# Kernel optimization log

Measured on AMD Instinct MI355X. Metric: run time of the kernel, lower is better.

Reference implementation:

```python
import jax, jax.numpy as jnp
import numpy as np

H, D, DS, CZ, S, B = 16, 24, 384, 128, 512, 1
EPS = 1e-5


def setup_inputs() -> dict:
    key = jax.random.key(0)
    ks = jax.random.split(key, 12)
    sc = lambda fan: 1.0 / np.sqrt(fan)
    inp = {
        's': jax.random.normal(ks[0], (B, S, DS), jnp.float32),
        'z': jax.random.normal(ks[1], (B, S, S, CZ), jnp.float32),
        'seq_mask': jnp.zeros((B, 1, 1, S), jnp.float32),
        'q_w': jax.random.normal(ks[2], (H * D, DS), jnp.float32) * sc(DS),
        'q_b': jax.random.normal(ks[3], (H * D,), jnp.float32) * 0.02,
        'k_w': jax.random.normal(ks[4], (H * D, DS), jnp.float32) * sc(DS),
        'v_w': jax.random.normal(ks[5], (H * D, DS), jnp.float32) * sc(DS),
        'g_w': jax.random.normal(ks[6], (H * D, DS), jnp.float32) * sc(DS),
        'o_w': jax.random.normal(ks[7], (DS, H * D), jnp.float32) * sc(H * D),
        'z_ln_w': jnp.ones((CZ,), jnp.float32),
        'z_ln_b': jnp.zeros((CZ,), jnp.float32),
        'z_w': jax.random.normal(ks[8], (H, CZ), jnp.float32) * sc(CZ),
    }
    return inp


def _layer_norm(x, w, b):
    mu = jnp.mean(x, axis=-1, keepdims=True)
    var = jnp.mean(jnp.square(x - mu), axis=-1, keepdims=True)
    return (x - mu) * jax.lax.rsqrt(var + EPS) * w + b


def reference(s, z, seq_mask, q_w, q_b, k_w, v_w, g_w, o_w, z_ln_w, z_ln_b, z_w):
    b, n, _ = s.shape
    # fused QKV projection (q has bias, k/v do not)
    q = (s @ q_w.T + q_b).reshape(b, n, H, D).transpose(0, 2, 1, 3)  # [B,H,S,D]
    k = (s @ k_w.T).reshape(b, n, H, D).transpose(0, 2, 1, 3)
    v = (s @ v_w.T).reshape(b, n, H, D).transpose(0, 2, 1, 3)
    # pair bias: layernorm(z) -> linear to H -> permute to [B,H,S,S]
    bias = _layer_norm(z, z_ln_w, z_ln_b) @ z_w.T          # [B,S,S,H]
    bias = bias.transpose(0, 3, 1, 2)                      # [B,H,S,S]
    bias = bias + seq_mask
    scores = jnp.einsum('bhqd,bhkd->bhqk', q, k) * (D ** -0.5) + bias
    attn = jax.nn.softmax(scores, axis=-1)
    o = jnp.einsum('bhqk,bhkd->bhqd', attn, v)             # [B,H,S,D]
    o = o.transpose(0, 2, 1, 3).reshape(b, n, H * D)
    g = jax.nn.sigmoid(s @ g_w.T)                          # gating
    return (o * g) @ o_w.T                                 # [B,S,DS]
```

## Files before the change

kernel.cpp:

```cpp
#include <hip/hip_runtime.h>

#define H 16
#define D 24
#define DS 384
#define CZ 128
#define S 512
#define EPSV 1e-5f

__global__ __launch_bounds__(256) void proj_kernel(
    const float* __restrict__ s, const float* __restrict__ q_w, const float* __restrict__ q_b,
    const float* __restrict__ k_w, const float* __restrict__ v_w, const float* __restrict__ g_w,
    float* __restrict__ Q, float* __restrict__ K, float* __restrict__ V, float* __restrict__ G)
{
    const int b = blockIdx.x;
    const int mat = b / 48;
    const int t = b % 48;
    const int by = t / 6, bx = t % 6;
    const float* w = (mat == 0) ? q_w : (mat == 1) ? k_w : (mat == 2) ? v_w : g_w;

    __shared__ float As[32][68];
    __shared__ float Ws[32][68];

    const int tid = threadIdx.x;
    const int tx = tid & 15, ty = tid >> 4;
    const int r8 = tid >> 3;
    const int c4 = tid & 7;

    float acc[4][4] = {};
    for (int kc = 0; kc < DS; kc += 32) {
        __syncthreads();
#pragma unroll
        for (int pass = 0; pass < 2; ++pass) {
            int r = r8 + pass * 32;
            float4 sv = *(const float4*)(s + (by * 64 + r) * DS + kc + c4 * 4);
            float4 wv = *(const float4*)(w + (bx * 64 + r) * DS + kc + c4 * 4);
            As[c4 * 4 + 0][r] = sv.x; As[c4 * 4 + 1][r] = sv.y;
            As[c4 * 4 + 2][r] = sv.z; As[c4 * 4 + 3][r] = sv.w;
            Ws[c4 * 4 + 0][r] = wv.x; Ws[c4 * 4 + 1][r] = wv.y;
            Ws[c4 * 4 + 2][r] = wv.z; Ws[c4 * 4 + 3][r] = wv.w;
        }
        __syncthreads();
#pragma unroll
        for (int k = 0; k < 32; ++k) {
            float4 a4 = *(const float4*)&As[k][ty * 4];
            float4 b4 = *(const float4*)&Ws[k][tx * 4];
            acc[0][0] += a4.x * b4.x; acc[0][1] += a4.x * b4.y; acc[0][2] += a4.x * b4.z; acc[0][3] += a4.x * b4.w;
            acc[1][0] += a4.y * b4.x; acc[1][1] += a4.y * b4.y; acc[1][2] += a4.y * b4.z; acc[1][3] += a4.y * b4.w;
            acc[2][0] += a4.z * b4.x; acc[2][1] += a4.z * b4.y; acc[2][2] += a4.z * b4.z; acc[2][3] += a4.z * b4.w;
            acc[3][0] += a4.w * b4.x; acc[3][1] += a4.w * b4.y; acc[3][2] += a4.w * b4.z; acc[3][3] += a4.w * b4.w;
        }
    }

    const int r0 = by * 64 + ty * 4;
    const int c0 = bx * 64 + tx * 4;
    float* dst = (mat == 0) ? Q : (mat == 1) ? K : (mat == 2) ? V : G;
#pragma unroll
    for (int ii = 0; ii < 4; ++ii) {
        float4 v;
        v.x = acc[ii][0]; v.y = acc[ii][1]; v.z = acc[ii][2]; v.w = acc[ii][3];
        if (mat == 0) {
            v.x += q_b[c0 + 0]; v.y += q_b[c0 + 1]; v.z += q_b[c0 + 2]; v.w += q_b[c0 + 3];
        } else if (mat == 3) {
            v.x = 1.f / (1.f + __expf(-v.x)); v.y = 1.f / (1.f + __expf(-v.y));
            v.z = 1.f / (1.f + __expf(-v.z)); v.w = 1.f / (1.f + __expf(-v.w));
        }
        *(float4*)(dst + (r0 + ii) * DS + c0) = v;
    }
}

__global__ __launch_bounds__(256) void score_kernel(
    const float* __restrict__ z, const float* __restrict__ seq_mask,
    const float* __restrict__ z_ln_w, const float* __restrict__ z_ln_b,
    const float* __restrict__ z_w,
    const float* __restrict__ Q, const float* __restrict__ K,
    float* __restrict__ scores)
{
    const int b = blockIdx.x;
    const int q = b >> 3;
    const int j0 = (b & 7) * 64;
    const int tid = threadIdx.x;
    const int w = tid >> 6;
    const int lane = tid & 63;

    __shared__ float a_s[H][CZ + 4];
    __shared__ float AhBh[2][H];
    __shared__ float qrow[DS];
    __shared__ float stats[4][2][68];
    __shared__ float opart[4][H][68];
    __shared__ float buf[H][68];

    {
        const int h = tid >> 4;
        const int c8 = (tid & 15) * 8;
        float A = 0.f, Bv = 0.f;
#pragma unroll
        for (int p = 0; p < 2; ++p) {
            float4 wz = *(const float4*)(z_w + h * CZ + c8 + p * 4);
            float4 lw = *(const float4*)(z_ln_w + c8 + p * 4);
            float4 lb = *(const float4*)(z_ln_b + c8 + p * 4);
            float4 a;
            a.x = lw.x * wz.x; a.y = lw.y * wz.y; a.z = lw.z * wz.z; a.w = lw.w * wz.w;
            *(float4*)&a_s[h][c8 + p * 4] = a;
            A += a.x + a.y + a.z + a.w;
            Bv += lb.x * wz.x + lb.y * wz.y + lb.z * wz.z + lb.w * wz.w;
        }
#pragma unroll
        for (int m = 1; m < 16; m <<= 1) {
            A += __shfl_xor(A, m);
            Bv += __shfl_xor(Bv, m);
        }
        if ((tid & 15) == 0) { AhBh[0][h] = A; AhBh[1][h] = Bv; }
    }
    for (int i = tid; i < DS; i += 256) qrow[i] = Q[q * DS + i];
    __syncthreads();

    {
        const int c0 = w * 32;
        const float* zr = z + ((long)q * S + j0 + lane) * CZ + c0;
        float4 zf[8];
#pragma unroll
        for (int t = 0; t < 8; ++t) zf[t] = *(const float4*)(zr + t * 4);

        float s1 = 0.f, s2 = 0.f;
#pragma unroll
        for (int t = 0; t < 8; ++t) {
            s1 += zf[t].x + zf[t].y + zf[t].z + zf[t].w;
            s2 += zf[t].x * zf[t].x + zf[t].y * zf[t].y + zf[t].z * zf[t].z + zf[t].w * zf[t].w;
        }
        stats[w][0][lane] = s1;
        stats[w][1][lane] = s2;

#pragma unroll
        for (int h = 0; h < H; ++h) {
            float acc = 0.f;
#pragma unroll
            for (int t = 0; t < 8; ++t) {
                float4 a4 = *(const float4*)&a_s[h][c0 + t * 4];
                acc += zf[t].x * a4.x + zf[t].y * a4.y + zf[t].z * a4.z + zf[t].w * a4.w;
            }
            opart[w][h][lane] = acc;
        }
    }
    __syncthreads();

    {
        const int r = tid >> 2;
        const int hq = tid & 3;
        float s1 = stats[0][0][r] + stats[1][0][r] + stats[2][0][r] + stats[3][0][r];
        float s2 = stats[0][1][r] + stats[1][1][r] + stats[2][1][r] + stats[3][1][r];
        const float mu = s1 * (1.f / 128.f);
        const float rs = rsqrtf(s2 * (1.f / 128.f) - mu * mu + EPSV);
        const float mk = seq_mask[j0 + r];
        const float scale = 0.2041241452319315f;
        const float* krow = K + (long)(j0 + r) * DS;

#pragma unroll
        for (int i = 0; i < 4; ++i) {
            const int h = hq * 4 + i;
            float dza = opart[0][h][r] + opart[1][h][r] + opart[2][h][r] + opart[3][h][r];
            const float4* k4 = (const float4*)(krow + h * D);
            const float4* q4 = (const float4*)(qrow + h * D);
            float qk = 0.f;
#pragma unroll
            for (int t = 0; t < 6; ++t) {
                float4 kv = k4[t];
                float4 qv = q4[t];
                qk += kv.x * qv.x + kv.y * qv.y + kv.z * qv.z + kv.w * qv.w;
            }
            const float bias = rs * dza - mu * rs * AhBh[0][h] + AhBh[1][h];
            buf[h][r] = qk * scale + bias + mk;
        }
    }
    __syncthreads();

    {
        const int h = tid >> 4, j4 = tid & 15;
        float4 v = *(const float4*)&buf[h][j4 * 4];
        *(float4*)(scores + ((q << 4) + h) * S + j0 + j4 * 4) = v;
    }
}

__global__ __launch_bounds__(256) void spv_kernel(
    const float* __restrict__ scores, const float* __restrict__ V,
    const float* __restrict__ G, float* __restrict__ og)
{
    const int q = blockIdx.x;
    const int tid = threadIdx.x;
    const int wv = tid >> 6;
    const int lane = tid & 63;

    __shared__ float sc[H][S + 4];
    __shared__ float opart[4][DS];
    __shared__ float inv_l[H];

    for (int i = tid; i < H * (S / 4); i += 256) {
        int row = i >> 7, f4 = i & 127;
        float4 v = ((const float4*)(scores + ((q << 4) + row) * S))[f4];
        *(float4*)&sc[row][f4 * 4] = v;
    }
    __syncthreads();

#pragma unroll
    for (int i = 0; i < 4; ++i) {
        int h = wv * 4 + i;
        float m = -1e30f;
        for (int j = lane; j < S; j += 64) m = fmaxf(m, sc[h][j]);
#pragma unroll
        for (int mk = 1; mk < 64; mk <<= 1) m = fmaxf(m, __shfl_xor(m, mk));
        float sum = 0.f;
        for (int j = lane; j < S; j += 64) {
            float p = __expf(sc[h][j] - m);
            sc[h][j] = p;
            sum += p;
        }
#pragma unroll
        for (int mk = 1; mk < 64; mk <<= 1) sum += __shfl_xor(sum, mk);
        if (lane == 0) inv_l[h] = 1.f / sum;
    }
    __syncthreads();

    {
        const int jb = wv * 128;
        const int c0 = lane * 4;
        const int h0 = c0 / 24;
        const int c1 = 256 + lane * 4;
        const int h1 = c1 / 24;
        float4 a0 = {0.f, 0.f, 0.f, 0.f};
        float4 a1 = {0.f, 0.f, 0.f, 0.f};
#pragma unroll 4
        for (int jj = 0; jj < 128; ++jj) {
            const int j = jb + jj;
            const float4* vr = (const float4*)(V + (long)j * DS);
            const float p0 = sc[h0][j];
            float4 v0 = vr[lane];
            a0.x += p0 * v0.x; a0.y += p0 * v0.y; a0.z += p0 * v0.z; a0.w += p0 * v0.w;
            if (lane < 32) {
                const float p1 = sc[h1][j];
                float4 v1 = vr[64 + lane];
                a1.x += p1 * v1.x; a1.y += p1 * v1.y; a1.z += p1 * v1.z; a1.w += p1 * v1.w;
            }
        }
        *(float4*)&opart[wv][c0] = a0;
        if (lane < 32) *(float4*)&opart[wv][c1] = a1;
    }
    __syncthreads();
    for (int i = tid; i < DS; i += 256) {
        float o = opart[0][i] + opart[1][i] + opart[2][i] + opart[3][i];
        int h = i / 24;
        og[q * DS + i] = o * inv_l[h] * G[q * DS + i];
    }
}

__global__ __launch_bounds__(256) void out_kernel(
    const float* __restrict__ og, const float* __restrict__ o_w, float* __restrict__ out)
{
    const int b = blockIdx.x;
    const int by = b / 6, bx = b % 6;

    __shared__ float As[32][68];
    __shared__ float Ws[32][68];

    const int tid = threadIdx.x;
    const int tx = tid & 15, ty = tid >> 4;
    const int r8 = tid >> 3;
    const int c4 = tid & 7;

    float acc[4][4] = {};
    for (int kc = 0; kc < DS; kc += 32) {
        __syncthreads();
#pragma unroll
        for (int pass = 0; pass < 2; ++pass) {
            int r = r8 + pass * 32;
            float4 sv = *(const float4*)(og + (by * 64 + r) * DS + kc + c4 * 4);
            float4 wvv = *(const float4*)(o_w + (bx * 64 + r) * DS + kc + c4 * 4);
            As[c4 * 4 + 0][r] = sv.x; As[c4 * 4 + 1][r] = sv.y;
            As[c4 * 4 + 2][r] = sv.z; As[c4 * 4 + 3][r] = sv.w;
            Ws[c4 * 4 + 0][r] = wvv.x; Ws[c4 * 4 + 1][r] = wvv.y;
            Ws[c4 * 4 + 2][r] = wvv.z; Ws[c4 * 4 + 3][r] = wvv.w;
        }
        __syncthreads();
#pragma unroll
        for (int k = 0; k < 32; ++k) {
            float4 a4 = *(const float4*)&As[k][ty * 4];
            float4 b4 = *(const float4*)&Ws[k][tx * 4];
            acc[0][0] += a4.x * b4.x; acc[0][1] += a4.x * b4.y; acc[0][2] += a4.x * b4.z; acc[0][3] += a4.x * b4.w;
            acc[1][0] += a4.y * b4.x; acc[1][1] += a4.y * b4.y; acc[1][2] += a4.y * b4.z; acc[1][3] += a4.y * b4.w;
            acc[2][0] += a4.z * b4.x; acc[2][1] += a4.z * b4.y; acc[2][2] += a4.z * b4.z; acc[2][3] += a4.z * b4.w;
            acc[3][0] += a4.w * b4.x; acc[3][1] += a4.w * b4.y; acc[3][2] += a4.w * b4.z; acc[3][3] += a4.w * b4.w;
        }
    }

    const int r0 = by * 64 + ty * 4;
    const int c0 = bx * 64 + tx * 4;
#pragma unroll
    for (int ii = 0; ii < 4; ++ii) {
        float4 v;
        v.x = acc[ii][0]; v.y = acc[ii][1]; v.z = acc[ii][2]; v.w = acc[ii][3];
        *(float4*)(out + (r0 + ii) * DS + c0) = v;
    }
}

extern "C" void kernel_launch(void* const* d_in, const int* in_sizes, int n_in,
                              void* d_out, int out_size, void* d_ws, size_t ws_size,
                              hipStream_t stream)
{
    const float* s      = (const float*)d_in[0];
    const float* z      = (const float*)d_in[1];
    const float* mask   = (const float*)d_in[2];
    const float* q_w    = (const float*)d_in[3];
    const float* q_b    = (const float*)d_in[4];
    const float* k_w    = (const float*)d_in[5];
    const float* v_w    = (const float*)d_in[6];
    const float* g_w    = (const float*)d_in[7];
    const float* o_w    = (const float*)d_in[8];
    const float* z_ln_w = (const float*)d_in[9];
    const float* z_ln_b = (const float*)d_in[10];
    const float* z_w    = (const float*)d_in[11];

    float* Q  = (float*)d_ws;
    float* K  = Q + S * DS;
    float* V  = K + S * DS;
    float* G  = V + S * DS;
    float* og = G + S * DS;
    float* scores = og + S * DS;

    hipLaunchKernelGGL(proj_kernel, dim3(192), dim3(256), 0, stream,
                       s, q_w, q_b, k_w, v_w, g_w, Q, K, V, G);
    hipLaunchKernelGGL(score_kernel, dim3(4096), dim3(256), 0, stream,
                       z, mask, z_ln_w, z_ln_b, z_w, Q, K, scores);
    hipLaunchKernelGGL(spv_kernel, dim3(S), dim3(256), 0, stream,
                       scores, V, G, og);
    hipLaunchKernelGGL(out_kernel, dim3(48), dim3(256), 0, stream,
                       og, o_w, (float*)d_out);
}
```

Measured before the change: 338.2 us.

## Restructure score kernel to stage z tiles in shared memory with register-blocked heads

The score kernel now handles 128 key rows per block instead of 64, halving the grid. Each block streams z through shared memory in 32-channel chunks. Each thread computes 4 heads for 2 rows, keeping the LN-folded weights in registers and accumulating layernorm statistics and the bias projection directly, so the cross-wave partial-sum reductions through shared memory go away. Q is read straight from global memory rather than staged. The kernel now needs more synchronisation per chunk and more registers, and the halved grid lowers parallelism.

```diff
diff --git a/kernel.cpp b/kernel.cpp
--- a/kernel.cpp
+++ b/kernel.cpp
@@ -76,18 +76,15 @@
     float* __restrict__ scores)
 {
     const int b = blockIdx.x;
-    const int q = b >> 3;
-    const int j0 = (b & 7) * 64;
+    const int q = b >> 2;
+    const int j0 = (b & 3) * 128;
     const int tid = threadIdx.x;
-    const int w = tid >> 6;
-    const int lane = tid & 63;
+    const int r = tid >> 2;
+    const int hq = tid & 3;
 
     __shared__ float a_s[H][CZ + 4];
     __shared__ float AhBh[2][H];
-    __shared__ float qrow[DS];
-    __shared__ float stats[4][2][68];
-    __shared__ float opart[4][H][68];
-    __shared__ float buf[H][68];
+    __shared__ float zs[128 * 36];
 
     {
         const int h = tid >> 4;
@@ -111,71 +108,105 @@
         }
         if ((tid & 15) == 0) { AhBh[0][h] = A; AhBh[1][h] = Bv; }
     }
-    for (int i = tid; i < DS; i += 256) qrow[i] = Q[q * DS + i];
-    __syncthreads();
-
-    {
-        const int c0 = w * 32;
-        const float* zr = z + ((long)q * S + j0 + lane) * CZ + c0;
-        float4 zf[8];
-#pragma unroll
-        for (int t = 0; t < 8; ++t) zf[t] = *(const float4*)(zr + t * 4);
-
-        float s1 = 0.f, s2 = 0.f;
-#pragma unroll
-        for (int t = 0; t < 8; ++t) {
-            s1 += zf[t].x + zf[t].y + zf[t].z + zf[t].w;
-            s2 += zf[t].x * zf[t].x + zf[t].y * zf[t].y + zf[t].z * zf[t].z + zf[t].w * zf[t].w;
-        }
-        stats[w][0][lane] = s1;
-        stats[w][1][lane] = s2;
-
-#pragma unroll
-        for (int h = 0; h < H; ++h) {
-            float acc = 0.f;
-#pragma unroll
-            for (int t = 0; t < 8; ++t) {
-                float4 a4 = *(const float4*)&a_s[h][c0 + t * 4];
-                acc += zf[t].x * a4.x + zf[t].y * a4.y + zf[t].z * a4.z + zf[t].w * a4.w;
+    __syncthreads();
+
+    float accz[2][4] = {};
+    float s1[2] = {0.f, 0.f}, s2[2] = {0.f, 0.f};
+    const float* zq = z + ((long)q * S + j0) * CZ;
+
+    for (int cc = 0; cc < 4; ++cc) {
+        const int c0 = cc * 32;
+#pragma unroll
+        for (int it = 0; it < 4; ++it) {
+            const int idx = it * 256 + tid;
+            const int row = idx >> 3, c8 = idx & 7;
+            float4 v = *(const float4*)(zq + (long)row * CZ + c0 + c8 * 4);
+            *(float4*)&zs[row * 36 + c8 * 4] = v;
+        }
+        __syncthreads();
+
+#pragma unroll
+        for (int sub = 0; sub < 2; ++sub) {
+            const int cb = sub * 16;
+            float4 areg[4][4];
+#pragma unroll
+            for (int i = 0; i < 4; ++i)
+#pragma unroll
+                for (int t = 0; t < 4; ++t)
+                    areg[i][t] = *(const float4*)&a_s[hq * 4 + i][c0 + cb + t * 4];
+
+#pragma unroll
+            for (int tl = 0; tl < 2; ++tl) {
+                const int row = tl * 64 + r;
+                float4 zf[4];
+#pragma unroll
+                for (int t = 0; t < 4; ++t)
+                    zf[t] = *(const float4*)&zs[row * 36 + cb + t * 4];
+#pragma unroll
+                for (int t = 0; t < 4; ++t) {
+                    s1[tl] += zf[t].x + zf[t].y + zf[t].z + zf[t].w;
+                    s2[tl] += zf[t].x * zf[t].x + zf[t].y * zf[t].y
+                            + zf[t].z * zf[t].z + zf[t].w * zf[t].w;
+                }
+#pragma unroll
+                for (int i = 0; i < 4; ++i) {
+                    accz[tl][i] += zf[0].x * areg[i][0].x + zf[0].y * areg[i][0].y
+                                 + zf[0].z * areg[i][0].z + zf[0].w * areg[i][0].w
+                                 + zf[1].x * areg[i][1].x + zf[1].y * areg[i][1].y
+                                 + zf[1].z * areg[i][1].z + zf[1].w * areg[i][1].w
+                                 + zf[2].x * areg[i][2].x + zf[2].y * areg[i][2].y
+                                 + zf[2].z * areg[i][2].z + zf[2].w * areg[i][2].w
+                                 + zf[3].x * areg[i][3].x + zf[3].y * areg[i][3].y
+                                 + zf[3].z * areg[i][3].z + zf[3].w * areg[i][3].w;
+                }
             }
-            opart[w][h][lane] = acc;
-        }
-    }
-    __syncthreads();
-
-    {
-        const int r = tid >> 2;
-        const int hq = tid & 3;
-        float s1 = stats[0][0][r] + stats[1][0][r] + stats[2][0][r] + stats[3][0][r];
-        float s2 = stats[0][1][r] + stats[1][1][r] + stats[2][1][r] + stats[3][1][r];
-        const float mu = s1 * (1.f / 128.f);
-        const float rs = rsqrtf(s2 * (1.f / 128.f) - mu * mu + EPSV);
-        const float mk = seq_mask[j0 + r];
-        const float scale = 0.2041241452319315f;
-        const float* krow = K + (long)(j0 + r) * DS;
-
+        }
+        __syncthreads();
+    }
+
+    float qk[2][4];
+#pragma unroll
+    for (int i = 0; i < 4; ++i) {
+        const int h = hq * 4 + i;
+        float4 qreg[6];
+#pragma unroll
+        for (int t = 0; t < 6; ++t)
+            qreg[t] = *(const float4*)(Q + q * DS + h * D + t * 4);
+#pragma unroll
+        for (int tl = 0; tl < 2; ++tl) {
+            const float4* kp = (const float4*)(K + (long)(j0 + tl * 64 + r) * DS + h * D);
+            float a = 0.f;
+#pragma unroll
+            for (int t = 0; t < 6; ++t) {
+                float4 kv = kp[t];
+                a += kv.x * qreg[t].x + kv.y * qreg[t].y + kv.z * qreg[t].z + kv.w * qreg[t].w;
+            }
+            qk[tl][i] = a;
+        }
+    }
+
+    float* buf = zs;
+    const float scale = 0.2041241452319315f;
+#pragma unroll
+    for (int tl = 0; tl < 2; ++tl) {
+        const int row = tl * 64 + r;
+        const float mu = s1[tl] * (1.f / 128.f);
+        const float rs = rsqrtf(s2[tl] * (1.f / 128.f) - mu * mu + EPSV);
+        const float mk = seq_mask[j0 + row];
 #pragma unroll
         for (int i = 0; i < 4; ++i) {
             const int h = hq * 4 + i;
-            float dza = opart[0][h][r] + opart[1][h][r] + opart[2][h][r] + opart[3][h][r];
-            const float4* k4 = (const float4*)(krow + h * D);
-            const float4* q4 = (const float4*)(qrow + h * D);
-            float qk = 0.f;
-#pragma unroll
-            for (int t = 0; t < 6; ++t) {
-                float4 kv = k4[t];
-                float4 qv = q4[t];
-                qk += kv.x * qv.x + kv.y * qv.y + kv.z * qv.z + kv.w * qv.w;
-            }
-            const float bias = rs * dza - mu * rs * AhBh[0][h] + AhBh[1][h];
-            buf[h][r] = qk * scale + bias + mk;
-        }
-    }
-    __syncthreads();
-
-    {
-        const int h = tid >> 4, j4 = tid & 15;
-        float4 v = *(const float4*)&buf[h][j4 * 4];
+            const float bias = rs * accz[tl][i] - mu * rs * AhBh[0][h] + AhBh[1][h];
+            buf[h * 132 + row] = qk[tl][i] * scale + bias + mk;
+        }
+    }
+    __syncthreads();
+
+#pragma unroll
+    for (int it = 0; it < 2; ++it) {
+        const int idx = it * 256 + tid;
+        const int h = idx >> 5, j4 = idx & 31;
+        float4 v = *(const float4*)&buf[h * 132 + j4 * 4];
         *(float4*)(scores + ((q << 4) + h) * S + j0 + j4 * 4) = v;
     }
 }
@@ -326,7 +357,7 @@
 
     hipLaunchKernelGGL(proj_kernel, dim3(192), dim3(256), 0, stream,
                        s, q_w, q_b, k_w, v_w, g_w, Q, K, V, G);
-    hipLaunchKernelGGL(score_kernel, dim3(4096), dim3(256), 0, stream,
+    hipLaunchKernelGGL(score_kernel, dim3(2048), dim3(256), 0, stream,
                        z, mask, z_ln_w, z_ln_b, z_w, Q, K, scores);
     hipLaunchKernelGGL(spv_kernel, dim3(S), dim3(256), 0, stream,
                        scores, V, G, og);
```

Result: slower. 383.8 us (+13.5%).

## Reduce pair-bias partial sums with wave shuffles instead of shared memory

Applied to the files above, without the earlier changes.

Reassigns work in the score kernel so the four lanes covering one z row sit together in a wave, each handling 32 channels. The layernorm statistics and per-head dot products are combined with xor shuffles, which removes the stats and opart shared arrays and one block barrier. Q is read straight from global memory instead of being staged in shared memory. The cost is 16 extra registers per thread for the per-head partials and a less coalesced z load pattern, since each lane now reads a 128-byte chunk from a different row.

```diff
diff --git a/kernel.cpp b/kernel.cpp
--- a/kernel.cpp
+++ b/kernel.cpp
@@ -81,12 +81,12 @@
     const int tid = threadIdx.x;
     const int w = tid >> 6;
     const int lane = tid & 63;
-
-    __shared__ float a_s[H][CZ + 4];
+    const int r = lane >> 2;
+    const int c = lane & 3;
+    const int row = w * 16 + r;
+
+    __shared__ float a_s[H][4][36];
     __shared__ float AhBh[2][H];
-    __shared__ float qrow[DS];
-    __shared__ float stats[4][2][68];
-    __shared__ float opart[4][H][68];
     __shared__ float buf[H][68];
 
     {
@@ -95,12 +95,13 @@
         float A = 0.f, Bv = 0.f;
 #pragma unroll
         for (int p = 0; p < 2; ++p) {
-            float4 wz = *(const float4*)(z_w + h * CZ + c8 + p * 4);
-            float4 lw = *(const float4*)(z_ln_w + c8 + p * 4);
-            float4 lb = *(const float4*)(z_ln_b + c8 + p * 4);
+            const int ch = c8 + p * 4;
+            float4 wz = *(const float4*)(z_w + h * CZ + ch);
+            float4 lw = *(const float4*)(z_ln_w + ch);
+            float4 lb = *(const float4*)(z_ln_b + ch);
             float4 a;
             a.x = lw.x * wz.x; a.y = lw.y * wz.y; a.z = lw.z * wz.z; a.w = lw.w * wz.w;
-            *(float4*)&a_s[h][c8 + p * 4] = a;
+            *(float4*)&a_s[h][ch >> 5][ch & 31] = a;
             A += a.x + a.y + a.z + a.w;
             Bv += lb.x * wz.x + lb.y * wz.y + lb.z * wz.z + lb.w * wz.w;
         }
@@ -111,65 +112,59 @@
         }
         if ((tid & 15) == 0) { AhBh[0][h] = A; AhBh[1][h] = Bv; }
     }
-    for (int i = tid; i < DS; i += 256) qrow[i] = Q[q * DS + i];
-    __syncthreads();
-
-    {
-        const int c0 = w * 32;
-        const float* zr = z + ((long)q * S + j0 + lane) * CZ + c0;
-        float4 zf[8];
-#pragma unroll
-        for (int t = 0; t < 8; ++t) zf[t] = *(const float4*)(zr + t * 4);
-
-        float s1 = 0.f, s2 = 0.f;
+    __syncthreads();
+
+    const float* zr = z + ((long)q * S + j0 + row) * CZ + c * 32;
+    float4 zf[8];
+#pragma unroll
+    for (int t = 0; t < 8; ++t) zf[t] = *(const float4*)(zr + t * 4);
+
+    float s1 = 0.f, s2 = 0.f;
+#pragma unroll
+    for (int t = 0; t < 8; ++t) {
+        s1 += zf[t].x + zf[t].y + zf[t].z + zf[t].w;
+        s2 += zf[t].x * zf[t].x + zf[t].y * zf[t].y + zf[t].z * zf[t].z + zf[t].w * zf[t].w;
+    }
+
+    float dza[H];
+#pragma unroll
+    for (int h = 0; h < H; ++h) {
+        float acc = 0.f;
 #pragma unroll
         for (int t = 0; t < 8; ++t) {
-            s1 += zf[t].x + zf[t].y + zf[t].z + zf[t].w;
-            s2 += zf[t].x * zf[t].x + zf[t].y * zf[t].y + zf[t].z * zf[t].z + zf[t].w * zf[t].w;
-        }
-        stats[w][0][lane] = s1;
-        stats[w][1][lane] = s2;
-
-#pragma unroll
-        for (int h = 0; h < H; ++h) {
-            float acc = 0.f;
-#pragma unroll
-            for (int t = 0; t < 8; ++t) {
-                float4 a4 = *(const float4*)&a_s[h][c0 + t * 4];
-                acc += zf[t].x * a4.x + zf[t].y * a4.y + zf[t].z * a4.z + zf[t].w * a4.w;
-            }
-            opart[w][h][lane] = acc;
-        }
-    }
-    __syncthreads();
-
-    {
-        const int r = tid >> 2;
-        const int hq = tid & 3;
-        float s1 = stats[0][0][r] + stats[1][0][r] + stats[2][0][r] + stats[3][0][r];
-        float s2 = stats[0][1][r] + stats[1][1][r] + stats[2][1][r] + stats[3][1][r];
-        const float mu = s1 * (1.f / 128.f);
-        const float rs = rsqrtf(s2 * (1.f / 128.f) - mu * mu + EPSV);
-        const float mk = seq_mask[j0 + r];
-        const float scale = 0.2041241452319315f;
-        const float* krow = K + (long)(j0 + r) * DS;
-
-#pragma unroll
-        for (int i = 0; i < 4; ++i) {
-            const int h = hq * 4 + i;
-            float dza = opart[0][h][r] + opart[1][h][r] + opart[2][h][r] + opart[3][h][r];
-            const float4* k4 = (const float4*)(krow + h * D);
-            const float4* q4 = (const float4*)(qrow + h * D);
-            float qk = 0.f;
-#pragma unroll
-            for (int t = 0; t < 6; ++t) {
-                float4 kv = k4[t];
-                float4 qv = q4[t];
-                qk += kv.x * qv.x + kv.y * qv.y + kv.z * qv.z + kv.w * qv.w;
-            }
-            const float bias = rs * dza - mu * rs * AhBh[0][h] + AhBh[1][h];
-            buf[h][r] = qk * scale + bias + mk;
-        }
+            float4 a4 = *(const float4*)&a_s[h][c][t * 4];
+            acc += zf[t].x * a4.x + zf[t].y * a4.y + zf[t].z * a4.z + zf[t].w * a4.w;
+        }
+        dza[h] = acc;
+    }
+
+#pragma unroll
+    for (int h = 0; h < H; ++h) {
+        dza[h] += __shfl_xor(dza[h], 1);
+        dza[h] += __shfl_xor(dza[h], 2);
+    }
+    s1 += __shfl_xor(s1, 1); s1 += __shfl_xor(s1, 2);
+    s2 += __shfl_xor(s2, 1); s2 += __shfl_xor(s2, 2);
+
+    const float mu = s1 * (1.f / 128.f);
+    const float rs = rsqrtf(s2 * (1.f / 128.f) - mu * mu + EPSV);
+    const float mk = seq_mask[j0 + row];
+
+    const float scale = 0.2041241452319315f;
+#pragma unroll
+    for (int i = 0; i < 4; ++i) {
+        const int h = c * 4 + i;
+        const float4* q4 = (const float4*)(Q + q * DS + h * D);
+        const float4* k4 = (const float4*)(K + (long)(j0 + row) * DS + h * D);
+        float qk = 0.f;
+#pragma unroll
+        for (int t = 0; t < 6; ++t) {
+            float4 qv = q4[t];
+            float4 kv = k4[t];
+            qk += kv.x * qv.x + kv.y * qv.y + kv.z * qv.z + kv.w * qv.w;
+        }
+        const float bias = rs * dza[h] - mu * rs * AhBh[0][h] + AhBh[1][h];
+        buf[h][row] = qk * scale + bias + mk;
     }
     __syncthreads();
 
```

Result: slower. 380.9 us (+12.6%).
